# Performance work log

Hardware: AMD Instinct MI355X
Metric: run time of the kernel (lower is better)

The kernel has to match this reference:

```python
import jax, jax.numpy as jnp
import numpy as np

B, I, H = 16384, 512, 512


def setup_inputs() -> dict:
    key = jax.random.key(0)
    ks = jax.random.split(key, 10)
    inputs = jax.random.normal(ks[0], (B, I), dtype=jnp.float32)
    state = jax.random.normal(ks[1], (B, 2 * H), dtype=jnp.float32)
    # xavier_uniform for w_ih: U(-a, a), a = sqrt(6 / (fan_in + fan_out))
    a = float(np.sqrt(6.0 / (2 * H + I)))
    w_ih = jax.random.uniform(ks[2], (2 * H, I), jnp.float32, -a, a)
    b_h = jnp.zeros((H,), jnp.float32)
    pi = float(np.pi)
    d1 = jax.random.uniform(ks[3], (H,), jnp.float32, -pi, pi)
    d2 = jax.random.uniform(ks[4], (H,), jnp.float32, -pi, pi)
    d3 = jax.random.uniform(ks[5], (H,), jnp.float32, -pi, pi)
    re1 = jax.random.uniform(ks[6], (H,), jnp.float32, -1.0, 1.0)
    im1 = jax.random.uniform(ks[7], (H,), jnp.float32, -1.0, 1.0)
    re2 = jax.random.uniform(ks[8], (H,), jnp.float32, -1.0, 1.0)
    im2 = jax.random.uniform(ks[9], (H,), jnp.float32, -1.0, 1.0)
    perm = jnp.asarray(np.random.default_rng(0).permutation(H), dtype=jnp.int32)
    return {"inputs": inputs, "state": state, "w_ih": w_ih, "b_h": b_h,
            "d1": d1, "d2": d2, "d3": d3,
            "re1": re1, "im1": im1, "re2": re2, "im2": im2, "perm": perm}


def _diag_mul(w, z):
    # multiply by exp(i*w) built as complex(cos w, sin w), as in the original
    return jax.lax.complex(jnp.cos(w), jnp.sin(w)) * z


def _reflect(re, im, z):
    # z - (2/||v||^2) * (z @ conj(v)) outer v   (faithful to original matmuls)
    v = jax.lax.complex(re, im)                 # [H]
    vz = z @ jnp.conj(v)                        # [B]
    factor = 2.0 / jnp.sum(re * re + im * im)   # real scalar
    return z - factor * vz[:, None] * v[None, :]


def _modrelu(z, b):
    norm = jnp.abs(z)
    scale = jax.nn.relu(norm + b) / (norm + 1e-6)
    return z * scale


def reference(inputs, state, w_ih, b_h, d1, d2, d3, re1, im1, re2, im2, perm):
    inputs_mul = inputs @ w_ih.T                                  # [B, 2H]
    z_in = jax.lax.complex(inputs_mul[:, :H], inputs_mul[:, H:])  # [B, H] c64
    state_c = jax.lax.complex(state[:, :H], state[:, H:])
    # Unitary chain (computed in original forward, but its result `preact` is
    # never used for the returned state -- faithfully reproduced).
    s = _diag_mul(d1, state_c)
    s = jnp.fft.fft(s, axis=-1)
    s = _reflect(re1, im1, s)
    s = s[:, perm]                 # column permutation (z.T[P].T)
    s = _diag_mul(d2, s)
    s = jnp.fft.ifft(s, axis=-1)
    s = _reflect(re2, im2, s)
    s = _diag_mul(d3, s)
    preact = z_in + s              # dead in original; kept for fidelity
    new_state_c = _modrelu(z_in, b_h)
    return jnp.concatenate([jnp.real(new_state_c), jnp.imag(new_state_c)], axis=1)
```

## Files before the change

### kernel.cpp

```cpp
#include <hip/hip_runtime.h>
#include <hip/hip_bf16.h>


typedef __attribute__((ext_vector_type(8))) short bf16x8;
typedef __attribute__((ext_vector_type(4))) float f32x4;

#define BM 128
#define BK 64
#define KDIM 512
#define NDIM 1024
#define NKT 8

#define VMCNT(n) asm volatile("s_waitcnt vmcnt(" #n ")" ::: "memory")
#define LGKM(n)  asm volatile("s_waitcnt lgkmcnt(" #n ")" ::: "memory")

__device__ __forceinline__ unsigned short f2bf(float f) {
    unsigned u = __builtin_bit_cast(unsigned, f);
    u += 0x7fffu + ((u >> 16) & 1u);
    return (unsigned short)(u >> 16);
}

__global__ __launch_bounds__(256) void cvt_both(
    const float* __restrict__ A, const float* __restrict__ W,
    unsigned short* __restrict__ Abf, unsigned short* __restrict__ Wbf,
    int nA4, int nTot4) {
    int i = blockIdx.x * blockDim.x + threadIdx.x;
    int stride = gridDim.x * blockDim.x;
    for (; i < nTot4; i += stride) {
        float4 v;
        if (i < nA4) v = reinterpret_cast<const float4*>(A)[i];
        else         v = reinterpret_cast<const float4*>(W)[i - nA4];
        ushort4 o;
        o.x = f2bf(v.x); o.y = f2bf(v.y); o.z = f2bf(v.z); o.w = f2bf(v.w);
        if (i < nA4) reinterpret_cast<ushort4*>(Abf)[i] = o;
        else         reinterpret_cast<ushort4*>(Wbf)[i - nA4] = o;
    }
}

__device__ __forceinline__ void gload_lds16(const void* g, void* l) {
    __builtin_amdgcn_global_load_lds(
        (const __attribute__((address_space(1))) unsigned int*)g,
        (__attribute__((address_space(3))) unsigned int*)l, 16, 0, 0);
}

__global__ __launch_bounds__(256, 2) void gemm_modrelu(
    const unsigned short* __restrict__ A,
    const unsigned short* __restrict__ W,
    const float* __restrict__ bh,
    float* __restrict__ out)
{
    __shared__ __align__(16) char smem[65536];
    unsigned short* At0 = (unsigned short*)smem;
    unsigned short* Bt0 = (unsigned short*)(smem + 32768);
    float* C = (float*)smem;

    const int tid = threadIdx.x;
    const int w   = tid >> 6;
    const int l   = tid & 63;
    const int l15 = l & 15;
    const int l4  = l >> 4;
    const int wm  = w >> 1;
    const int wn  = w & 1;

    const int bx = blockIdx.x;
    const int lg = (bx & 7) * 128 + (bx >> 3);
    const int mb = lg >> 3;
    const int cb = lg & 7;

    const int srow = l >> 3;
    const int sseg = (l & 7) ^ srow;
    const unsigned short* ga[4];
    const unsigned short* gb[4];
    int ldso[4];
#pragma unroll
    for (int is = 0; is < 4; ++is) {
        int row  = w * 32 + is * 8 + srow;
        ga[is]   = A + (size_t)(mb * BM + row) * KDIM + sseg * 8;
        int wrow = (row >> 6) * 512 + cb * 64 + (row & 63);
        gb[is]   = W + (size_t)wrow * KDIM + sseg * 8;
        ldso[is] = (w * 32 + is * 8) * BK;
    }

    auto stage = [&](int kt, int buf) {
        unsigned short* at = At0 + buf * (BM * BK);
        unsigned short* bt = Bt0 + buf * (BM * BK);
#pragma unroll
        for (int is = 0; is < 4; ++is)
            gload_lds16(ga[is] + kt * BK, at + ldso[is]);
#pragma unroll
        for (int is = 0; is < 4; ++is)
            gload_lds16(gb[is] + kt * BK, bt + ldso[is]);
    };

    f32x4 acc[4][4];
#pragma unroll
    for (int i = 0; i < 4; ++i)
#pragma unroll
        for (int j = 0; j < 4; ++j) acc[i][j] = f32x4{0.f, 0.f, 0.f, 0.f};

    stage(0, 0);
    stage(1, 1);
    VMCNT(8);
    __builtin_amdgcn_s_barrier();

#pragma unroll
    for (int kt = 0; kt < NKT; ++kt) {
        const int buf = kt & 1;
        const unsigned short* at = At0 + buf * (BM * BK);
        const unsigned short* bt = Bt0 + buf * (BM * BK);

#pragma unroll
        for (int ks = 0; ks < 2; ++ks) {
            bf16x8 af[4], bf[4];
#pragma unroll
            for (int i = 0; i < 4; ++i) {
                int row = wm * 64 + i * 16 + l15;
                af[i] = *(const bf16x8*)(&at[row * BK + (((ks * 4 + l4) ^ (row & 7)) * 8)]);
            }
#pragma unroll
            for (int j = 0; j < 4; ++j) {
                int row = (j >> 1) * 64 + wn * 32 + (j & 1) * 16 + l15;
                bf[j] = *(const bf16x8*)(&bt[row * BK + (((ks * 4 + l4) ^ (row & 7)) * 8)]);
            }
            LGKM(0);
            __builtin_amdgcn_sched_barrier(0);
            __builtin_amdgcn_s_setprio(1);
#pragma unroll
            for (int i = 0; i < 4; ++i)
#pragma unroll
                for (int j = 0; j < 4; ++j)
                    acc[i][j] = __builtin_amdgcn_mfma_f32_16x16x32_bf16(
                        af[i], bf[j], acc[i][j], 0, 0, 0);
            __builtin_amdgcn_s_setprio(0);
        }

        if (kt + 1 < NKT) {
            __builtin_amdgcn_s_barrier();
            if (kt + 2 < NKT) {
                stage(kt + 2, buf);
                VMCNT(8);
            } else {
                VMCNT(0);
            }
            __builtin_amdgcn_s_barrier();
        }
    }

    __syncthreads();
#pragma unroll
    for (int j = 0; j < 2; ++j) {
        int col = wn * 32 + j * 16 + l15;
        float b = bh[cb * 64 + col];
#pragma unroll
        for (int i = 0; i < 4; ++i) {
#pragma unroll
            for (int jj = 0; jj < 4; ++jj) {
                int rowl = wm * 64 + i * 16 + l4 * 4 + jj;
                float re  = acc[i][j][jj];
                float imv = acc[i][j + 2][jj];
                float norm  = sqrtf(re * re + imv * imv);
                float scale = fmaxf(norm + b, 0.f) * __builtin_amdgcn_rcpf(norm + 1e-6f);
                C[rowl * 128 + col]      = re  * scale;
                C[rowl * 128 + 64 + col] = imv * scale;
            }
        }
    }
    __syncthreads();

    const int seg   = l & 31;
    const int rhalf = l >> 5;
#pragma unroll
    for (int it = 0; it < 16; ++it) {
        int rowl = w * 32 + it * 2 + rhalf;
        f32x4 v = *reinterpret_cast<const f32x4*>(&C[rowl * 128 + seg * 4]);
        size_t m = (size_t)(mb * BM + rowl);
        int n = (seg < 16) ? (cb * 64 + seg * 4)
                           : (512 + cb * 64 + (seg - 16) * 4);
        __builtin_nontemporal_store(v, reinterpret_cast<f32x4*>(out + m * NDIM + n));
    }
}

extern "C" void kernel_launch(void* const* d_in, const int* in_sizes, int n_in,
                              void* d_out, int out_size, void* d_ws, size_t ws_size,
                              hipStream_t stream) {
    const float* inputs = (const float*)d_in[0];
    const float* w_ih   = (const float*)d_in[2];
    const float* b_h    = (const float*)d_in[3];
    float* out = (float*)d_out;

    unsigned short* Abf = (unsigned short*)d_ws;
    unsigned short* Wbf = (unsigned short*)((char*)d_ws + (size_t)16384 * 512 * 2);

    const int nA4 = (16384 * 512) / 4;
    const int nW4 = (1024 * 512) / 4;
    cvt_both<<<2048, 256, 0, stream>>>(inputs, w_ih, Abf, Wbf, nA4, nA4 + nW4);

    gemm_modrelu<<<1024, 256, 0, stream>>>(Abf, Wbf, b_h, out);
}
```

Baseline: 42.54 us.

## Double GEMM M-tile to 256 rows with BK 32 and two-pass epilogue

```diff
diff --git a/kernel.cpp b/kernel.cpp
--- a/kernel.cpp
+++ b/kernel.cpp
@@ -5,11 +5,12 @@
 typedef __attribute__((ext_vector_type(8))) short bf16x8;
 typedef __attribute__((ext_vector_type(4))) float f32x4;
 
-#define BM 128
-#define BK 64
+#define BM 256
+#define BK 32
 #define KDIM 512
 #define NDIM 1024
-#define NKT 8
+#define NKT 16
+#define CSTR 132
 
 #define VMCNT(n) asm volatile("s_waitcnt vmcnt(" #n ")" ::: "memory")
 #define LGKM(n)  asm volatile("s_waitcnt lgkmcnt(" #n ")" ::: "memory")
@@ -49,10 +50,10 @@
     const float* __restrict__ bh,
     float* __restrict__ out)
 {
-    __shared__ __align__(16) char smem[65536];
+    __shared__ __align__(16) char smem[67584];
     unsigned short* At0 = (unsigned short*)smem;
     unsigned short* Bt0 = (unsigned short*)(smem + 32768);
-    float* C = (float*)smem;
+    float* Cf = (float*)smem;
 
     const int tid = threadIdx.x;
     const int w   = tid >> 6;
@@ -63,82 +64,79 @@
     const int wn  = w & 1;
 
     const int bx = blockIdx.x;
-    const int lg = (bx & 7) * 128 + (bx >> 3);
+    const int lg = (bx & 7) * 64 + (bx >> 3);
     const int mb = lg >> 3;
     const int cb = lg & 7;
 
-    const int srow = l >> 3;
-    const int sseg = (l & 7) ^ srow;
+    const int r4   = tid >> 2;
+    const int sgr  = (tid & 3) ^ ((r4 >> 1) & 3);
     const unsigned short* ga[4];
-    const unsigned short* gb[4];
-    int ldso[4];
-#pragma unroll
-    for (int is = 0; is < 4; ++is) {
-        int row  = w * 32 + is * 8 + srow;
-        ga[is]   = A + (size_t)(mb * BM + row) * KDIM + sseg * 8;
-        int wrow = (row >> 6) * 512 + cb * 64 + (row & 63);
-        gb[is]   = W + (size_t)wrow * KDIM + sseg * 8;
-        ldso[is] = (w * 32 + is * 8) * BK;
+    const unsigned short* gbp[2];
+#pragma unroll
+    for (int is = 0; is < 4; ++is)
+        ga[is] = A + (size_t)(mb * BM + is * 64 + r4) * KDIM + sgr * 8;
+#pragma unroll
+    for (int is = 0; is < 2; ++is) {
+        int r    = is * 64 + r4;
+        int wrow = (r >> 6) * 512 + cb * 64 + (r & 63);
+        gbp[is]  = W + (size_t)wrow * KDIM + sgr * 8;
     }
 
     auto stage = [&](int kt, int buf) {
-        unsigned short* at = At0 + buf * (BM * BK);
-        unsigned short* bt = Bt0 + buf * (BM * BK);
 #pragma unroll
         for (int is = 0; is < 4; ++is)
-            gload_lds16(ga[is] + kt * BK, at + ldso[is]);
-#pragma unroll
-        for (int is = 0; is < 4; ++is)
-            gload_lds16(gb[is] + kt * BK, bt + ldso[is]);
+            gload_lds16(ga[is] + kt * BK, At0 + buf * 8192 + is * 2048 + w * 512);
+#pragma unroll
+        for (int is = 0; is < 2; ++is)
+            gload_lds16(gbp[is] + kt * BK, Bt0 + buf * 4096 + is * 2048 + w * 512);
     };
 
-    f32x4 acc[4][4];
-#pragma unroll
-    for (int i = 0; i < 4; ++i)
+    f32x4 acc[8][4];
+#pragma unroll
+    for (int i = 0; i < 8; ++i)
 #pragma unroll
         for (int j = 0; j < 4; ++j) acc[i][j] = f32x4{0.f, 0.f, 0.f, 0.f};
 
     stage(0, 0);
     stage(1, 1);
-    VMCNT(8);
+    VMCNT(6);
     __builtin_amdgcn_s_barrier();
+
+    const int ag = (l4 ^ ((l15 >> 1) & 3)) * 8;
 
 #pragma unroll
     for (int kt = 0; kt < NKT; ++kt) {
         const int buf = kt & 1;
-        const unsigned short* at = At0 + buf * (BM * BK);
-        const unsigned short* bt = Bt0 + buf * (BM * BK);
-
-#pragma unroll
-        for (int ks = 0; ks < 2; ++ks) {
-            bf16x8 af[4], bf[4];
-#pragma unroll
-            for (int i = 0; i < 4; ++i) {
-                int row = wm * 64 + i * 16 + l15;
-                af[i] = *(const bf16x8*)(&at[row * BK + (((ks * 4 + l4) ^ (row & 7)) * 8)]);
-            }
-#pragma unroll
-            for (int j = 0; j < 4; ++j) {
-                int row = (j >> 1) * 64 + wn * 32 + (j & 1) * 16 + l15;
-                bf[j] = *(const bf16x8*)(&bt[row * BK + (((ks * 4 + l4) ^ (row & 7)) * 8)]);
-            }
-            LGKM(0);
-            __builtin_amdgcn_sched_barrier(0);
-            __builtin_amdgcn_s_setprio(1);
-#pragma unroll
-            for (int i = 0; i < 4; ++i)
-#pragma unroll
-                for (int j = 0; j < 4; ++j)
-                    acc[i][j] = __builtin_amdgcn_mfma_f32_16x16x32_bf16(
-                        af[i], bf[j], acc[i][j], 0, 0, 0);
-            __builtin_amdgcn_s_setprio(0);
-        }
+        const unsigned short* at = At0 + buf * 8192;
+        const unsigned short* bt = Bt0 + buf * 4096;
+
+        bf16x8 af[8], bfr[4];
+#pragma unroll
+        for (int i = 0; i < 8; ++i) {
+            int row = wm * 128 + i * 16 + l15;
+            af[i] = *(const bf16x8*)(&at[row * 32 + ag]);
+        }
+#pragma unroll
+        for (int j = 0; j < 4; ++j) {
+            int row = wn * 64 + j * 16 + l15;
+            bfr[j] = *(const bf16x8*)(&bt[row * 32 + ag]);
+        }
+        LGKM(0);
+        __builtin_amdgcn_sched_barrier(0);
+        __builtin_amdgcn_s_setprio(1);
+#pragma unroll
+        for (int i = 0; i < 8; ++i)
+#pragma unroll
+            for (int j = 0; j < 4; ++j)
+                acc[i][j] = __builtin_amdgcn_mfma_f32_16x16x32_bf16(
+                    af[i], bfr[j], acc[i][j], 0, 0, 0);
+        __builtin_amdgcn_s_setprio(0);
 
         if (kt + 1 < NKT) {
             __builtin_amdgcn_s_barrier();
             if (kt + 2 < NKT) {
                 stage(kt + 2, buf);
-                VMCNT(8);
+                VMCNT(6);
             } else {
                 VMCNT(0);
             }
@@ -146,37 +144,44 @@
         }
     }
 
-    __syncthreads();
-#pragma unroll
-    for (int j = 0; j < 2; ++j) {
-        int col = wn * 32 + j * 16 + l15;
-        float b = bh[cb * 64 + col];
-#pragma unroll
-        for (int i = 0; i < 4; ++i) {
-#pragma unroll
-            for (int jj = 0; jj < 4; ++jj) {
-                int rowl = wm * 64 + i * 16 + l4 * 4 + jj;
-                float re  = acc[i][j][jj];
-                float imv = acc[i][j + 2][jj];
-                float norm  = sqrtf(re * re + imv * imv);
-                float scale = fmaxf(norm + b, 0.f) * __builtin_amdgcn_rcpf(norm + 1e-6f);
-                C[rowl * 128 + col]      = re  * scale;
-                C[rowl * 128 + 64 + col] = imv * scale;
+    const int srow16 = tid >> 4;
+    const int s      = tid & 15;
+    const f32x4 bhv  = *reinterpret_cast<const f32x4*>(&bh[cb * 64 + s * 4]);
+
+#pragma unroll
+    for (int h = 0; h < 2; ++h) {
+        __syncthreads();
+        if (wm == h) {
+#pragma unroll
+            for (int i = 0; i < 8; ++i)
+#pragma unroll
+                for (int j = 0; j < 4; ++j)
+#pragma unroll
+                    for (int jj = 0; jj < 4; ++jj)
+                        Cf[(i * 16 + l4 * 4 + jj) * CSTR + wn * 64 + j * 16 + l15]
+                            = acc[i][j][jj];
+        }
+        __syncthreads();
+#pragma unroll
+        for (int sw = 0; sw < 8; ++sw) {
+            int rl = sw * 16 + srow16;
+            f32x4 re = *reinterpret_cast<const f32x4*>(&Cf[rl * CSTR + s * 4]);
+            f32x4 im = *reinterpret_cast<const f32x4*>(&Cf[rl * CSTR + 64 + s * 4]);
+            f32x4 ore, oim;
+#pragma unroll
+            for (int e = 0; e < 4; ++e) {
+                float norm  = sqrtf(re[e] * re[e] + im[e] * im[e]);
+                float scale = fmaxf(norm + bhv[e], 0.f) *
+                              __builtin_amdgcn_rcpf(norm + 1e-6f);
+                ore[e] = re[e] * scale;
+                oim[e] = im[e] * scale;
             }
-        }
-    }
-    __syncthreads();
-
-    const int seg   = l & 31;
-    const int rhalf = l >> 5;
-#pragma unroll
-    for (int it = 0; it < 16; ++it) {
-        int rowl = w * 32 + it * 2 + rhalf;
-        f32x4 v = *reinterpret_cast<const f32x4*>(&C[rowl * 128 + seg * 4]);
-        size_t m = (size_t)(mb * BM + rowl);
-        int n = (seg < 16) ? (cb * 64 + seg * 4)
-                           : (512 + cb * 64 + (seg - 16) * 4);
-        __builtin_nontemporal_store(v, reinterpret_cast<f32x4*>(out + m * NDIM + n));
+            size_t m = (size_t)(mb * BM + h * 128 + rl);
+            __builtin_nontemporal_store(ore,
+                reinterpret_cast<f32x4*>(out + m * NDIM + cb * 64 + s * 4));
+            __builtin_nontemporal_store(oim,
+                reinterpret_cast<f32x4*>(out + m * NDIM + 512 + cb * 64 + s * 4));
+        }
     }
 }
 
@@ -195,5 +200,5 @@
     const int nW4 = (1024 * 512) / 4;
     cvt_both<<<2048, 256, 0, stream>>>(inputs, w_ih, Abf, Wbf, nA4, nA4 + nW4);
 
-    gemm_modrelu<<<1024, 256, 0, stream>>>(Abf, Wbf, b_h, out);
-}
+    gemm_modrelu<<<512, 256, 0, stream>>>(Abf, Wbf, b_h, out);
+}
```

Measured after the change: 44.05 us. 3.5% more time.
